# Performance work log

Hardware: AMD Instinct MI355X
Metric: run time of the kernel (lower is better)

Reference implementation:

```python
import jax, jax.numpy as jnp
import numpy as np
import math

B, S, D, V = 16, 512, 64, 32000
MAX_SEQ = 512
TEMP = 1.0
EPS = 1e-12


def setup_inputs() -> dict:
    key = jax.random.key(0)
    k0, k1, k2, k3, k4 = jax.random.split(key, 5)
    tokens = jax.random.randint(k0, (B, S), 0, V)
    token_emb = jax.random.normal(k1, (V, D), dtype=jnp.float32) * 0.02
    lin_w1 = jax.random.normal(k2, (D, D), dtype=jnp.float32) * (1.0 / math.sqrt(D))
    lin_w2 = jax.random.normal(k3, (D, D), dtype=jnp.float32) * (1.0 / math.sqrt(D))
    edge_scale = jnp.full((1,), 0.1, dtype=jnp.float32)  # nn.Parameter init 0.1
    out_w = jax.random.normal(k4, (V, D), dtype=jnp.float32) * 0.02
    return {"tokens": tokens, "token_emb": token_emb, "lin_w1": lin_w1,
            "lin_w2": lin_w2, "edge_scale": edge_scale, "out_w": out_w}


def _embed(tokens, token_emb):
    # polar positional components (seq_len <= max_seq_len branch)
    pos = jnp.arange(S, dtype=jnp.float32)
    thetas = 2.0 * math.pi * (pos / MAX_SEQ)
    rs = 0.3 + 0.6 * (pos / (MAX_SEQ - 1))
    e0 = (rs * jnp.cos(thetas))[None, :, None]          # [1,S,1]
    e1 = (rs * jnp.sin(thetas))[None, :, None]          # [1,S,1]
    tok = token_emb[tokens][:, :, : D - 2]              # [B,S,D-2]
    emb = jnp.concatenate([jnp.broadcast_to(e0, (tok.shape[0], S, 1)),
                           jnp.broadcast_to(e1, (tok.shape[0], S, 1)),
                           tok], axis=-1)               # [B,S,D]
    norms = jnp.sqrt(jnp.clip(jnp.einsum('bsd,bsd->bs', emb, emb), EPS, None))
    return emb / norms[:, :, None]


def _attention(emb):
    # pairwise Euclidean distance attention, diagonal distance zeroed
    n2 = jnp.einsum('bsd,bsd->bs', emb, emb)                      # [B,S]
    dots = jnp.einsum('bqd,bkd->bqk', emb, emb)                   # [B,S,S]
    sq = n2[:, :, None] + n2[:, None, :] - 2.0 * dots
    dist = jnp.sqrt(jnp.clip(sq, EPS, None))
    dist = dist * (1.0 - jnp.eye(S, dtype=dist.dtype))[None]      # eye_mask
    return jax.nn.softmax(-dist / TEMP, axis=-1)                  # [B,S,S]


def reference(tokens, token_emb, lin_w1, lin_w2, edge_scale, out_w):
    emb = _embed(tokens, token_emb)            # [B,S,D]
    attn = _attention(emb)                     # [B,S,S]
    h = emb
    for w in (lin_w1, lin_w2):
        # message passing: x_j -> lin(x_j), edge weight = attn * edge_scale,
        # scatter-add over all incoming edges == batched attn @ h
        h = edge_scale[0] * jnp.einsum('bqk,bkd->bqd', attn, h @ w.T)
    logits = jnp.einsum('bsd,vd->bsv', h, out_w)   # [B,S,V]
    return logits
```

## Files before the change

### kernel.cpp

```cpp
#include <hip/hip_runtime.h>
#include <hip/hip_bf16.h>


#define S_ 512
#define D_ 64
#define V_ 32000

typedef __attribute__((ext_vector_type(8))) __bf16 bf16x8;
typedef __attribute__((ext_vector_type(4))) float f32x4;

__device__ inline unsigned short f2bf(float x) {
    __hip_bfloat16 h = __float2bfloat16(x);
    return __builtin_bit_cast(unsigned short, h);
}

__global__ __launch_bounds__(256) void embed_kernel(const int* __restrict__ tokens,
                                                    const float* __restrict__ temb,
                                                    float* __restrict__ emb,
                                                    float* __restrict__ n2) {
    int row  = blockIdx.x * 4 + (threadIdx.x >> 6);
    int lane = threadIdx.x & 63;
    int s    = row & (S_ - 1);
    int tok  = tokens[row];
    float val;
    if (lane < 2) {
        float fs    = (float)s;
        float theta = 6.283185307179586f * (fs * (1.0f / 512.0f));
        float r     = 0.3f + 0.6f * (fs * (1.0f / 511.0f));
        val = (lane == 0) ? r * cosf(theta) : r * sinf(theta);
    } else {
        val = temb[tok * D_ + lane - 2];
    }
    float ss = val * val;
#pragma unroll
    for (int off = 32; off; off >>= 1) ss += __shfl_xor(ss, off, 64);
    float nrm = sqrtf(fmaxf(ss, 1e-12f));
    float e   = val / nrm;
    emb[row * D_ + lane] = e;
    float nn = e * e;
#pragma unroll
    for (int off = 32; off; off >>= 1) nn += __shfl_xor(nn, off, 64);
    if (lane == 0) n2[row] = nn;
}

__global__ __launch_bounds__(256) void attn_kernel(const float* __restrict__ emb,
                                                   const float* __restrict__ n2,
                                                   float* __restrict__ attn) {
    __shared__ float qs[16][68];
    __shared__ float ks[64][68];
    __shared__ float sc[16][520];
    __shared__ float n2qs[16];
    __shared__ float n2ks[64];
    int b  = blockIdx.x >> 5;
    int q0 = (blockIdx.x & 31) * 16;
    int t  = threadIdx.x;
    const float* ebase = emb + (size_t)b * S_ * D_;
    {
        int r = t >> 4, c4 = (t & 15) * 4;
        *reinterpret_cast<float4*>(&qs[r][c4]) =
            *reinterpret_cast<const float4*>(&ebase[(q0 + r) * D_ + c4]);
    }
    if (t < 16) n2qs[t] = n2[b * S_ + q0 + t];

    int qh = t >> 5;
    int kh = t & 31;

    for (int kt = 0; kt < 8; ++kt) {
        int k0 = kt * 64;
        __syncthreads();
#pragma unroll
        for (int j = 0; j < 4; ++j) {
            int f4 = t + j * 256;
            int r = f4 >> 4, c4 = (f4 & 15) * 4;
            *reinterpret_cast<float4*>(&ks[r][c4]) =
                *reinterpret_cast<const float4*>(&ebase[(k0 + r) * D_ + c4]);
        }
        if (t < 64) n2ks[t] = n2[b * S_ + k0 + t];
        __syncthreads();

        f32x4 acc[2][2];
#pragma unroll
        for (int i = 0; i < 2; ++i)
#pragma unroll
            for (int j = 0; j < 2; ++j) acc[i][j] = (f32x4){0.f, 0.f, 0.f, 0.f};
#pragma unroll
        for (int dc = 0; dc < 16; ++dc) {
            f32x4 qv0 = *reinterpret_cast<f32x4*>(&qs[2 * qh][dc * 4]);
            f32x4 qv1 = *reinterpret_cast<f32x4*>(&qs[2 * qh + 1][dc * 4]);
            f32x4 kv0 = *reinterpret_cast<f32x4*>(&ks[kh][dc * 4]);
            f32x4 kv1 = *reinterpret_cast<f32x4*>(&ks[kh + 32][dc * 4]);
            acc[0][0] += qv0 * kv0; acc[0][1] += qv0 * kv1;
            acc[1][0] += qv1 * kv0; acc[1][1] += qv1 * kv1;
        }
#pragma unroll
        for (int i = 0; i < 2; ++i)
#pragma unroll
            for (int j = 0; j < 2; ++j) {
                int q = 2 * qh + i, k = kh + 32 * j;
                f32x4 a = acc[i][j];
                float dot = (a[0] + a[1]) + (a[2] + a[3]);
                float sq  = n2qs[q] + n2ks[k] - 2.0f * dot;
                float sv  = (q0 + q == k0 + k) ? 0.0f : -sqrtf(fmaxf(sq, 1e-12f));
                sc[q][k0 + k] = sv;
            }
    }
    __syncthreads();
    int wave = t >> 6, lane = t & 63;
    for (int r = 0; r < 4; ++r) {
        int q = wave * 4 + r;
        float ex[8];
        float sum = 0.f;
#pragma unroll
        for (int i = 0; i < 8; ++i) {
            ex[i] = expf(sc[q][lane + i * 64]);
            sum += ex[i];
        }
#pragma unroll
        for (int off = 32; off; off >>= 1) sum += __shfl_xor(sum, off, 64);
        float inv = 1.0f / sum;
#pragma unroll
        for (int i = 0; i < 8; ++i)
            attn[((size_t)(b * S_ + q0 + q)) * S_ + lane + i * 64] = ex[i] * inv;
    }
}

__global__ __launch_bounds__(256) void proj_kernel(const float* __restrict__ h,
                                                   const float* __restrict__ w,
                                                   float* __restrict__ out) {
    __shared__ float ws[64][68];
    __shared__ float hs[16][68];
    int t  = threadIdx.x;
    int r0 = blockIdx.x * 16;
#pragma unroll
    for (int j = 0; j < 4; ++j) {
        int f4 = t + j * 256;
        int r = f4 >> 4, c4 = (f4 & 15) * 4;
        *reinterpret_cast<float4*>(&ws[r][c4]) =
            *reinterpret_cast<const float4*>(&w[r * D_ + c4]);
    }
    {
        int r = t >> 4, c4 = (t & 15) * 4;
        *reinterpret_cast<float4*>(&hs[r][c4]) =
            *reinterpret_cast<const float4*>(&h[(r0 + r) * D_ + c4]);
    }
    __syncthreads();
    int q = t >> 4, dh = t & 15;
    f32x4 acc[4];
#pragma unroll
    for (int dj = 0; dj < 4; ++dj) acc[dj] = (f32x4){0.f, 0.f, 0.f, 0.f};
#pragma unroll
    for (int ec = 0; ec < 16; ++ec) {
        f32x4 hv = *reinterpret_cast<f32x4*>(&hs[q][ec * 4]);
#pragma unroll
        for (int dj = 0; dj < 4; ++dj) {
            f32x4 wv = *reinterpret_cast<f32x4*>(&ws[dh * 4 + dj][ec * 4]);
            acc[dj] += hv * wv;
        }
    }
    float4 r;
    r.x = (acc[0][0] + acc[0][1]) + (acc[0][2] + acc[0][3]);
    r.y = (acc[1][0] + acc[1][1]) + (acc[1][2] + acc[1][3]);
    r.z = (acc[2][0] + acc[2][1]) + (acc[2][2] + acc[2][3]);
    r.w = (acc[3][0] + acc[3][1]) + (acc[3][2] + acc[3][3]);
    *reinterpret_cast<float4*>(&out[(r0 + q) * D_ + dh * 4]) = r;
}

template <bool BF16OUT>
__global__ __launch_bounds__(256) void prop_kernel(const float* __restrict__ attn,
                                                   const float* __restrict__ tmat,
                                                   const float* __restrict__ edge_scale,
                                                   float* __restrict__ outf,
                                                   unsigned short* __restrict__ outb) {
    __shared__ float As[16][68];
    __shared__ float Ts[64][68];
    int b  = blockIdx.x >> 5;
    int q0 = (blockIdx.x & 31) * 16;
    int t  = threadIdx.x;
    int q = t >> 4, dh = t & 15;
    f32x4 acc = (f32x4){0.f, 0.f, 0.f, 0.f};
    const float* abase = attn + ((size_t)b * S_ + q0) * S_;
    const float* tbase = tmat + (size_t)b * S_ * D_;
    for (int kt = 0; kt < 8; ++kt) {
        int k0 = kt * 64;
        __syncthreads();
        {
            int r = t >> 4, c4 = (t & 15) * 4;
            *reinterpret_cast<float4*>(&As[r][c4]) =
                *reinterpret_cast<const float4*>(&abase[(size_t)r * S_ + k0 + c4]);
        }
#pragma unroll
        for (int j = 0; j < 4; ++j) {
            int f4 = t + j * 256;
            int r = f4 >> 4, c4 = (f4 & 15) * 4;
            *reinterpret_cast<float4*>(&Ts[r][c4]) =
                *reinterpret_cast<const float4*>(&tbase[(k0 + r) * D_ + c4]);
        }
        __syncthreads();
#pragma unroll
        for (int kc = 0; kc < 16; ++kc) {
            f32x4 av = *reinterpret_cast<f32x4*>(&As[q][kc * 4]);
#pragma unroll
            for (int ks = 0; ks < 4; ++ks) {
                f32x4 tv = *reinterpret_cast<f32x4*>(&Ts[kc * 4 + ks][dh * 4]);
                acc += av[ks] * tv;
            }
        }
    }
    float scale = edge_scale[0];
    size_t rowbase = ((size_t)(b * S_ + q0 + q)) * D_ + dh * 4;
    if (BF16OUT) {
        ushort4 r;
        r.x = f2bf(scale * acc[0]); r.y = f2bf(scale * acc[1]);
        r.z = f2bf(scale * acc[2]); r.w = f2bf(scale * acc[3]);
        *reinterpret_cast<ushort4*>(&outb[rowbase]) = r;
    } else {
        *reinterpret_cast<float4*>(&outf[rowbase]) =
            make_float4(scale * acc[0], scale * acc[1], scale * acc[2], scale * acc[3]);
    }
}

__global__ __launch_bounds__(256) void cast_kernel(const float* __restrict__ in,
                                                   unsigned short* __restrict__ out, int n) {
    int i = (blockIdx.x * 256 + threadIdx.x) * 4;
    if (i >= n) return;
    float4 v = *reinterpret_cast<const float4*>(in + i);
    ushort4 r;
    r.x = f2bf(v.x); r.y = f2bf(v.y); r.z = f2bf(v.z); r.w = f2bf(v.w);
    *reinterpret_cast<ushort4*>(out + i) = r;
}

__global__ __launch_bounds__(256) void logits_kernel(const unsigned short* __restrict__ hb,
                                                     const unsigned short* __restrict__ wb,
                                                     float* __restrict__ out) {
    int bid = blockIdx.x;
    int nt = bid % 250, mt = bid / 250;
    int n0 = nt * 128, m0 = mt * 128;
    int wave = threadIdx.x >> 6, lane = threadIdx.x & 63;
    int nw = n0 + wave * 32;
    int lr = lane & 15, lh = lane >> 4;

    bf16x8 a[2][2];
#pragma unroll
    for (int ns = 0; ns < 2; ++ns)
#pragma unroll
        for (int kh = 0; kh < 2; ++kh)
            a[ns][kh] = *reinterpret_cast<const bf16x8*>(
                wb + (size_t)(nw + ns * 16 + lr) * D_ + kh * 32 + lh * 8);

    bf16x8 bfr[8][2];
#pragma unroll
    for (int ms = 0; ms < 8; ++ms)
#pragma unroll
        for (int kh = 0; kh < 2; ++kh)
            bfr[ms][kh] = *reinterpret_cast<const bf16x8*>(
                hb + (size_t)(m0 + ms * 16 + lr) * D_ + kh * 32 + lh * 8);

    f32x4 acc[2][8];
#pragma unroll
    for (int ns = 0; ns < 2; ++ns)
#pragma unroll
        for (int ms = 0; ms < 8; ++ms)
            acc[ns][ms] = (f32x4){0.f, 0.f, 0.f, 0.f};

#pragma unroll
    for (int ns = 0; ns < 2; ++ns)
#pragma unroll
        for (int ms = 0; ms < 8; ++ms) {
            acc[ns][ms] = __builtin_amdgcn_mfma_f32_16x16x32_bf16(a[ns][0], bfr[ms][0], acc[ns][ms], 0, 0, 0);
            acc[ns][ms] = __builtin_amdgcn_mfma_f32_16x16x32_bf16(a[ns][1], bfr[ms][1], acc[ns][ms], 0, 0, 0);
        }

#pragma unroll
    for (int ns = 0; ns < 2; ++ns) {
        int colbase = nw + ns * 16 + lh * 4;
#pragma unroll
        for (int ms = 0; ms < 8; ++ms) {
            int row = m0 + ms * 16 + lr;
            f32x4 v = acc[ns][ms];
            *reinterpret_cast<float4*>(out + (size_t)row * V_ + colbase) =
                make_float4(v[0], v[1], v[2], v[3]);
        }
    }
}

extern "C" void kernel_launch(void* const* d_in, const int* in_sizes, int n_in,
                              void* d_out, int out_size, void* d_ws, size_t ws_size,
                              hipStream_t stream) {
    const int*   tokens = (const int*)d_in[0];
    const float* temb   = (const float*)d_in[1];
    const float* w1     = (const float*)d_in[2];
    const float* w2     = (const float*)d_in[3];
    const float* escale = (const float*)d_in[4];
    const float* outw   = (const float*)d_in[5];
    float*       out    = (float*)d_out;

    char* tail = (char*)d_out + 1048576000ull - 23068672ull;
    float* attn = (float*)(tail);
    float* emb  = (float*)(tail + 16777216);
    float* t1   = (float*)(tail + 18874368);
    float* h1   = (float*)(tail + 20971520);

    char* ws = (char*)d_ws;
    unsigned short* hb = (unsigned short*)(ws);
    unsigned short* wb = (unsigned short*)(ws + 1048576);
    float*          n2 = (float*)(ws + 5144576);

    embed_kernel<<<2048, 256, 0, stream>>>(tokens, temb, emb, n2);
    attn_kernel<<<512, 256, 0, stream>>>(emb, n2, attn);
    cast_kernel<<<2000, 256, 0, stream>>>(outw, wb, V_ * D_);
    proj_kernel<<<512, 256, 0, stream>>>(emb, w1, t1);
    prop_kernel<false><<<512, 256, 0, stream>>>(attn, t1, escale, h1, nullptr);
    proj_kernel<<<512, 256, 0, stream>>>(h1, w2, t1);
    prop_kernel<true><<<512, 256, 0, stream>>>(attn, t1, escale, nullptr, hb);
    logits_kernel<<<16000, 256, 0, stream>>>(hb, wb, out);
}
```

Baseline: 347.2 us.

## Enlarge attn/prop register tiles and stage logits output through LDS

The attention and propagation kernels now use 32-query tiles with 128 threads and 4x4 register blocking, raising arithmetic reuse per LDS load and vectorising the softmax reads and writes. The logits kernel writes its MFMA results into a shared-memory tile and then stores full 512-byte row segments, so global writes coalesce instead of being scattered 16-byte pieces. The trade-offs are half as many blocks for the small kernels, which lowers parallelism on a large GPU, and about 67KB of extra LDS plus a barrier in the logits kernel, which may reduce its occupancy.

```diff
diff --git a/kernel.cpp b/kernel.cpp
--- a/kernel.cpp
+++ b/kernel.cpp
@@ -43,34 +43,36 @@
     if (lane == 0) n2[row] = nn;
 }
 
-__global__ __launch_bounds__(256) void attn_kernel(const float* __restrict__ emb,
+__global__ __launch_bounds__(128) void attn_kernel(const float* __restrict__ emb,
                                                    const float* __restrict__ n2,
                                                    float* __restrict__ attn) {
-    __shared__ float qs[16][68];
+    __shared__ float qs[32][68];
     __shared__ float ks[64][68];
-    __shared__ float sc[16][520];
-    __shared__ float n2qs[16];
+    __shared__ float sc[32][520];
+    __shared__ float n2qs[32];
     __shared__ float n2ks[64];
-    int b  = blockIdx.x >> 5;
-    int q0 = (blockIdx.x & 31) * 16;
+    int b  = blockIdx.x >> 4;
+    int q0 = (blockIdx.x & 15) * 32;
     int t  = threadIdx.x;
     const float* ebase = emb + (size_t)b * S_ * D_;
-    {
-        int r = t >> 4, c4 = (t & 15) * 4;
+#pragma unroll
+    for (int j = 0; j < 4; ++j) {
+        int f4 = t + j * 128;
+        int r = f4 >> 4, c4 = (f4 & 15) * 4;
         *reinterpret_cast<float4*>(&qs[r][c4]) =
             *reinterpret_cast<const float4*>(&ebase[(q0 + r) * D_ + c4]);
     }
-    if (t < 16) n2qs[t] = n2[b * S_ + q0 + t];
-
-    int qh = t >> 5;
-    int kh = t & 31;
+    if (t < 32) n2qs[t] = n2[b * S_ + q0 + t];
+
+    int qg = t >> 4;
+    int kg = t & 15;
 
     for (int kt = 0; kt < 8; ++kt) {
         int k0 = kt * 64;
         __syncthreads();
 #pragma unroll
-        for (int j = 0; j < 4; ++j) {
-            int f4 = t + j * 256;
+        for (int j = 0; j < 8; ++j) {
+            int f4 = t + j * 128;
             int r = f4 >> 4, c4 = (f4 & 15) * 4;
             *reinterpret_cast<float4*>(&ks[r][c4]) =
                 *reinterpret_cast<const float4*>(&ebase[(k0 + r) * D_ + c4]);
@@ -78,25 +80,28 @@
         if (t < 64) n2ks[t] = n2[b * S_ + k0 + t];
         __syncthreads();
 
-        f32x4 acc[2][2];
-#pragma unroll
-        for (int i = 0; i < 2; ++i)
-#pragma unroll
-            for (int j = 0; j < 2; ++j) acc[i][j] = (f32x4){0.f, 0.f, 0.f, 0.f};
+        f32x4 acc[4][4];
+#pragma unroll
+        for (int i = 0; i < 4; ++i)
+#pragma unroll
+            for (int j = 0; j < 4; ++j) acc[i][j] = (f32x4){0.f, 0.f, 0.f, 0.f};
 #pragma unroll
         for (int dc = 0; dc < 16; ++dc) {
-            f32x4 qv0 = *reinterpret_cast<f32x4*>(&qs[2 * qh][dc * 4]);
-            f32x4 qv1 = *reinterpret_cast<f32x4*>(&qs[2 * qh + 1][dc * 4]);
-            f32x4 kv0 = *reinterpret_cast<f32x4*>(&ks[kh][dc * 4]);
-            f32x4 kv1 = *reinterpret_cast<f32x4*>(&ks[kh + 32][dc * 4]);
-            acc[0][0] += qv0 * kv0; acc[0][1] += qv0 * kv1;
-            acc[1][0] += qv1 * kv0; acc[1][1] += qv1 * kv1;
-        }
-#pragma unroll
-        for (int i = 0; i < 2; ++i)
-#pragma unroll
-            for (int j = 0; j < 2; ++j) {
-                int q = 2 * qh + i, k = kh + 32 * j;
+            f32x4 qv[4], kv[4];
+#pragma unroll
+            for (int i = 0; i < 4; ++i) qv[i] = *reinterpret_cast<f32x4*>(&qs[qg * 4 + i][dc * 4]);
+#pragma unroll
+            for (int j = 0; j < 4; ++j) kv[j] = *reinterpret_cast<f32x4*>(&ks[kg * 4 + j][dc * 4]);
+#pragma unroll
+            for (int i = 0; i < 4; ++i)
+#pragma unroll
+                for (int j = 0; j < 4; ++j) acc[i][j] += qv[i] * kv[j];
+        }
+#pragma unroll
+        for (int i = 0; i < 4; ++i)
+#pragma unroll
+            for (int j = 0; j < 4; ++j) {
+                int q = qg * 4 + i, k = kg * 4 + j;
                 f32x4 a = acc[i][j];
                 float dot = (a[0] + a[1]) + (a[2] + a[3]);
                 float sq  = n2qs[q] + n2ks[k] - 2.0f * dot;
@@ -106,21 +111,23 @@
     }
     __syncthreads();
     int wave = t >> 6, lane = t & 63;
-    for (int r = 0; r < 4; ++r) {
-        int q = wave * 4 + r;
-        float ex[8];
-        float sum = 0.f;
-#pragma unroll
-        for (int i = 0; i < 8; ++i) {
-            ex[i] = expf(sc[q][lane + i * 64]);
-            sum += ex[i];
-        }
+    for (int r = 0; r < 16; ++r) {
+        int q = wave * 16 + r;
+        f32x4 ex0, ex1;
+        f32x4 v0 = *reinterpret_cast<f32x4*>(&sc[q][lane * 4]);
+        f32x4 v1 = *reinterpret_cast<f32x4*>(&sc[q][256 + lane * 4]);
+#pragma unroll
+        for (int i = 0; i < 4; ++i) { ex0[i] = expf(v0[i]); ex1[i] = expf(v1[i]); }
+        float sum = (ex0[0] + ex0[1]) + (ex0[2] + ex0[3]) +
+                    (ex1[0] + ex1[1]) + (ex1[2] + ex1[3]);
 #pragma unroll
         for (int off = 32; off; off >>= 1) sum += __shfl_xor(sum, off, 64);
         float inv = 1.0f / sum;
-#pragma unroll
-        for (int i = 0; i < 8; ++i)
-            attn[((size_t)(b * S_ + q0 + q)) * S_ + lane + i * 64] = ex[i] * inv;
+        float* row = attn + ((size_t)(b * S_ + q0 + q)) * S_;
+        *reinterpret_cast<float4*>(row + lane * 4) =
+            make_float4(ex0[0] * inv, ex0[1] * inv, ex0[2] * inv, ex0[3] * inv);
+        *reinterpret_cast<float4*>(row + 256 + lane * 4) =
+            make_float4(ex1[0] * inv, ex1[1] * inv, ex1[2] * inv, ex1[3] * inv);
     }
 }
 
@@ -166,31 +173,35 @@
 }
 
 template <bool BF16OUT>
-__global__ __launch_bounds__(256) void prop_kernel(const float* __restrict__ attn,
+__global__ __launch_bounds__(128) void prop_kernel(const float* __restrict__ attn,
                                                    const float* __restrict__ tmat,
                                                    const float* __restrict__ edge_scale,
                                                    float* __restrict__ outf,
                                                    unsigned short* __restrict__ outb) {
-    __shared__ float As[16][68];
+    __shared__ float As[32][68];
     __shared__ float Ts[64][68];
-    int b  = blockIdx.x >> 5;
-    int q0 = (blockIdx.x & 31) * 16;
+    int b  = blockIdx.x >> 4;
+    int q0 = (blockIdx.x & 15) * 32;
     int t  = threadIdx.x;
-    int q = t >> 4, dh = t & 15;
-    f32x4 acc = (f32x4){0.f, 0.f, 0.f, 0.f};
+    int qg = t >> 4, dh = t & 15;
+    f32x4 acc[4];
+#pragma unroll
+    for (int i = 0; i < 4; ++i) acc[i] = (f32x4){0.f, 0.f, 0.f, 0.f};
     const float* abase = attn + ((size_t)b * S_ + q0) * S_;
     const float* tbase = tmat + (size_t)b * S_ * D_;
     for (int kt = 0; kt < 8; ++kt) {
         int k0 = kt * 64;
         __syncthreads();
-        {
-            int r = t >> 4, c4 = (t & 15) * 4;
+#pragma unroll
+        for (int j = 0; j < 4; ++j) {
+            int f4 = t + j * 128;
+            int r = f4 >> 4, c4 = (f4 & 15) * 4;
             *reinterpret_cast<float4*>(&As[r][c4]) =
                 *reinterpret_cast<const float4*>(&abase[(size_t)r * S_ + k0 + c4]);
         }
 #pragma unroll
-        for (int j = 0; j < 4; ++j) {
-            int f4 = t + j * 256;
+        for (int j = 0; j < 8; ++j) {
+            int f4 = t + j * 128;
             int r = f4 >> 4, c4 = (f4 & 15) * 4;
             *reinterpret_cast<float4*>(&Ts[r][c4]) =
                 *reinterpret_cast<const float4*>(&tbase[(k0 + r) * D_ + c4]);
@@ -198,24 +209,32 @@
         __syncthreads();
 #pragma unroll
         for (int kc = 0; kc < 16; ++kc) {
-            f32x4 av = *reinterpret_cast<f32x4*>(&As[q][kc * 4]);
-#pragma unroll
-            for (int ks = 0; ks < 4; ++ks) {
-                f32x4 tv = *reinterpret_cast<f32x4*>(&Ts[kc * 4 + ks][dh * 4]);
-                acc += av[ks] * tv;
+            f32x4 tv[4];
+#pragma unroll
+            for (int ks = 0; ks < 4; ++ks)
+                tv[ks] = *reinterpret_cast<f32x4*>(&Ts[kc * 4 + ks][dh * 4]);
+#pragma unroll
+            for (int i = 0; i < 4; ++i) {
+                f32x4 av = *reinterpret_cast<f32x4*>(&As[qg * 4 + i][kc * 4]);
+#pragma unroll
+                for (int ks = 0; ks < 4; ++ks) acc[i] += av[ks] * tv[ks];
             }
         }
     }
     float scale = edge_scale[0];
-    size_t rowbase = ((size_t)(b * S_ + q0 + q)) * D_ + dh * 4;
-    if (BF16OUT) {
-        ushort4 r;
-        r.x = f2bf(scale * acc[0]); r.y = f2bf(scale * acc[1]);
-        r.z = f2bf(scale * acc[2]); r.w = f2bf(scale * acc[3]);
-        *reinterpret_cast<ushort4*>(&outb[rowbase]) = r;
-    } else {
-        *reinterpret_cast<float4*>(&outf[rowbase]) =
-            make_float4(scale * acc[0], scale * acc[1], scale * acc[2], scale * acc[3]);
+#pragma unroll
+    for (int i = 0; i < 4; ++i) {
+        size_t rowbase = ((size_t)(b * S_ + q0 + qg * 4 + i)) * D_ + dh * 4;
+        if (BF16OUT) {
+            ushort4 r;
+            r.x = f2bf(scale * acc[i][0]); r.y = f2bf(scale * acc[i][1]);
+            r.z = f2bf(scale * acc[i][2]); r.w = f2bf(scale * acc[i][3]);
+            *reinterpret_cast<ushort4*>(&outb[rowbase]) = r;
+        } else {
+            *reinterpret_cast<float4*>(&outf[rowbase]) =
+                make_float4(scale * acc[i][0], scale * acc[i][1],
+                            scale * acc[i][2], scale * acc[i][3]);
+        }
     }
 }
 
@@ -232,11 +251,12 @@
 __global__ __launch_bounds__(256) void logits_kernel(const unsigned short* __restrict__ hb,
                                                      const unsigned short* __restrict__ wb,
                                                      float* __restrict__ out) {
+    __shared__ float Ct[128][132];
     int bid = blockIdx.x;
     int nt = bid % 250, mt = bid / 250;
     int n0 = nt * 128, m0 = mt * 128;
     int wave = threadIdx.x >> 6, lane = threadIdx.x & 63;
-    int nw = n0 + wave * 32;
+    int nw = wave * 32;
     int lr = lane & 15, lh = lane >> 4;
 
     bf16x8 a[2][2];
@@ -245,7 +265,7 @@
 #pragma unroll
         for (int kh = 0; kh < 2; ++kh)
             a[ns][kh] = *reinterpret_cast<const bf16x8*>(
-                wb + (size_t)(nw + ns * 16 + lr) * D_ + kh * 32 + lh * 8);
+                wb + (size_t)(n0 + nw + ns * 16 + lr) * D_ + kh * 32 + lh * 8);
 
     bf16x8 bfr[8][2];
 #pragma unroll
@@ -271,15 +291,22 @@
         }
 
 #pragma unroll
-    for (int ns = 0; ns < 2; ++ns) {
-        int colbase = nw + ns * 16 + lh * 4;
+    for (int ns = 0; ns < 2; ++ns)
 #pragma unroll
         for (int ms = 0; ms < 8; ++ms) {
-            int row = m0 + ms * 16 + lr;
             f32x4 v = acc[ns][ms];
-            *reinterpret_cast<float4*>(out + (size_t)row * V_ + colbase) =
+            *reinterpret_cast<float4*>(&Ct[ms * 16 + lr][nw + ns * 16 + lh * 4]) =
                 make_float4(v[0], v[1], v[2], v[3]);
         }
+    __syncthreads();
+
+    int t = threadIdx.x;
+    int r8 = t >> 5, c = (t & 31) * 4;
+#pragma unroll
+    for (int j = 0; j < 16; ++j) {
+        int row = r8 + j * 8;
+        *reinterpret_cast<float4*>(out + (size_t)(m0 + row) * V_ + n0 + c) =
+            *reinterpret_cast<float4*>(&Ct[row][c]);
     }
 }
 
@@ -306,11 +333,11 @@
     float*          n2 = (float*)(ws + 5144576);
 
     embed_kernel<<<2048, 256, 0, stream>>>(tokens, temb, emb, n2);
-    attn_kernel<<<512, 256, 0, stream>>>(emb, n2, attn);
+    attn_kernel<<<256, 128, 0, stream>>>(emb, n2, attn);
     cast_kernel<<<2000, 256, 0, stream>>>(outw, wb, V_ * D_);
     proj_kernel<<<512, 256, 0, stream>>>(emb, w1, t1);
-    prop_kernel<false><<<512, 256, 0, stream>>>(attn, t1, escale, h1, nullptr);
+    prop_kernel<false><<<256, 128, 0, stream>>>(attn, t1, escale, h1, nullptr);
     proj_kernel<<<512, 256, 0, stream>>>(h1, w2, t1);
-    prop_kernel<true><<<512, 256, 0, stream>>>(attn, t1, escale, nullptr, hb);
+    prop_kernel<true><<<256, 128, 0, stream>>>(attn, t1, escale, nullptr, hb);
     logits_kernel<<<16000, 256, 0, stream>>>(hb, wb, out);
 }
```

Result: slower. 356.4 us (+2.6%).
